# Optimization experiments

Hardware: AMD Instinct MI355X
Metric: run time of the kernel (lower is better)

## Reference

```python
import jax, jax.numpy as jnp
import numpy as np

D_MODEL = 1024
N_HEADS = 16
HEAD_DIM = D_MODEL // N_HEADS
MAX_LEN = 2048
BATCH = 2
SEQ = 2048


def setup_inputs() -> dict:
    key = jax.random.key(0)
    ks = jax.random.split(key, 6)
    std = 1.0 / np.sqrt(D_MODEL)
    x = jax.random.normal(ks[0], (BATCH, SEQ, D_MODEL), dtype=jnp.float32)
    Wqkv = jax.random.uniform(ks[1], (D_MODEL, 3 * D_MODEL), minval=-std, maxval=std, dtype=jnp.float32)
    bqkv = jax.random.uniform(ks[2], (3 * D_MODEL,), minval=-std, maxval=std, dtype=jnp.float32)
    Wout = jax.random.uniform(ks[3], (D_MODEL, D_MODEL), minval=-std, maxval=std, dtype=jnp.float32)
    bout = jax.random.uniform(ks[4], (D_MODEL,), minval=-std, maxval=std, dtype=jnp.float32)
    rel_pos_bias = 0.02 * jax.random.normal(ks[5], (2 * MAX_LEN - 1,), dtype=jnp.float32)
    return {"x": x, "Wqkv": Wqkv, "bqkv": bqkv, "Wout": Wout, "bout": bout, "rel_pos_bias": rel_pos_bias}


def reference(x, Wqkv, bqkv, Wout, bout, rel_pos_bias):
    B, S, _ = x.shape
    scale = HEAD_DIM ** -0.5
    qkv = x @ Wqkv + bqkv                       # [B,S,3*dm]
    qkv = qkv.reshape(B, S, 3, N_HEADS, HEAD_DIM)
    qkv = jnp.transpose(qkv, (2, 0, 3, 1, 4))   # [3,B,H,S,D]
    q, k, v = qkv[0], qkv[1], qkv[2]
    scores = jnp.einsum('bhqd,bhkd->bhqk', q, k) * scale
    pos = jnp.arange(S)
    rel = jnp.clip(pos[:, None] - pos[None, :] + (MAX_LEN - 1), 0, 2 * MAX_LEN - 2)
    scores = scores + rel_pos_bias[rel][None, None]  # bias shared over batch & heads
    probs = jax.nn.softmax(scores, axis=-1)
    out = jnp.einsum('bhqk,bhkd->bhqd', probs, v)    # [B,H,S,D]
    out = jnp.transpose(out, (0, 2, 1, 3)).reshape(B, S, D_MODEL)
    return out @ Wout + bout
```

## Files before the change

kernel.cpp:

```cpp
#include <hip/hip_runtime.h>
#include <cmath>

#define B_ 2
#define S_ 2048
#define H_ 16
#define D_ 64
#define DM 1024

typedef unsigned short u16;
using short8 = __attribute__((ext_vector_type(8))) short;
using f32x4  = __attribute__((ext_vector_type(4))) float;
using f32x16 = __attribute__((ext_vector_type(16))) float;
using i32x4  = __attribute__((ext_vector_type(4))) int;

__device__ __forceinline__ u16 f32_to_bf16(float f) {
    unsigned int u = __float_as_uint(f);
    u += 0x7fffu + ((u >> 16) & 1u);
    return (u16)(u >> 16);
}

__device__ __forceinline__ float exp2_fast(float x) {
    float r;
    asm("v_exp_f32 %0, %1" : "=v"(r) : "v"(x));
    return r;
}

__device__ __forceinline__ int cvt_pk_bf16(float lo, float hi) {
    int r;
    asm("v_cvt_pk_bf16_f32 %0, %1, %2" : "=v"(r) : "v"(lo), "v"(hi));
    return r;
}

__device__ __forceinline__ void gl_lds16(const void* src, void* dst) {
    __builtin_amdgcn_global_load_lds(
        (const __attribute__((address_space(1))) unsigned int*)src,
        (__attribute__((address_space(3))) unsigned int*)dst, 16, 0, 0);
}

__device__ __forceinline__ f32x16 mfma32(short8 a, short8 b, f32x16 c) {
    return __builtin_amdgcn_mfma_f32_32x32x16_bf16(a, b, c, 0, 0, 0);
}

__global__ __launch_bounds__(256) void relattn_prep(
    const float* __restrict__ x, const float* __restrict__ Wqkv,
    const float* __restrict__ Wout, const float* __restrict__ relb,
    u16* __restrict__ xb, u16* __restrict__ WqkvT, u16* __restrict__ WoutT,
    float* __restrict__ relb2)
{
    __shared__ float T[64][65];
    const int tid = threadIdx.x;
    int blk = blockIdx.x;
    if (blk >= 3072) {
        int i0 = ((blk - 3072) * 256 + tid) * 4;
#pragma unroll
        for (int j = 0; j < 4; ++j)
            if (i0 + j < 2 * 2048 - 1)
                relb2[i0 + j] = relb[i0 + j] * 1.44269504f;
        return;
    }
    if (blk < 2048) {
        size_t base = ((size_t)blk * 256 + tid) * 8;
        float4 v0 = *(const float4*)(x + base);
        float4 v1 = *(const float4*)(x + base + 4);
        ushort4 p0 = make_ushort4(f32_to_bf16(v0.x), f32_to_bf16(v0.y),
                                  f32_to_bf16(v0.z), f32_to_bf16(v0.w));
        ushort4 p1 = make_ushort4(f32_to_bf16(v1.x), f32_to_bf16(v1.y),
                                  f32_to_bf16(v1.z), f32_to_bf16(v1.w));
        *(ushort4*)(xb + base) = p0;
        *(ushort4*)(xb + base + 4) = p1;
        return;
    }
    int id = blk - 2048;
    const float* in; u16* outp; int R, C;
    if (id < 768) { in = Wqkv; outp = WqkvT; R = 1024; C = 3072; }
    else          { id -= 768; in = Wout;  outp = WoutT; R = 1024; C = 1024; }
    const int tpr = C >> 6;
    const int r0 = (id / tpr) << 6, c0 = (id % tpr) << 6;
#pragma unroll
    for (int it = 0; it < 4; ++it) {
        int e = tid + it * 256;
        int row = e >> 4, c4 = (e & 15) << 2;
        float4 v = *(const float4*)(in + (size_t)(r0 + row) * C + c0 + c4);
        T[row][c4 + 0] = v.x; T[row][c4 + 1] = v.y;
        T[row][c4 + 2] = v.z; T[row][c4 + 3] = v.w;
    }
    __syncthreads();
#pragma unroll
    for (int it = 0; it < 4; ++it) {
        int e = tid + it * 256;
        int crow = e >> 4, r4 = (e & 15) << 2;
        ushort4 pk = make_ushort4(f32_to_bf16(T[r4 + 0][crow]), f32_to_bf16(T[r4 + 1][crow]),
                                  f32_to_bf16(T[r4 + 2][crow]), f32_to_bf16(T[r4 + 3][crow]));
        *(ushort4*)(outp + (size_t)(c0 + crow) * R + r0 + r4) = pk;
    }
}

__global__ __launch_bounds__(256) void relattn_gemm_qkv(
    const u16* __restrict__ A, const u16* __restrict__ Bm,
    const float* __restrict__ bias, u16* __restrict__ qk, u16* __restrict__ Vt)
{
    __shared__ alignas(16) unsigned char AsB[16384];
    __shared__ alignas(16) unsigned char BsB[16384];
    const int tid = threadIdx.x;
    const int w = tid >> 6, l = tid & 63, ln = l & 15, hi = l >> 4;
    const int wr = w >> 1, wc = w & 1;
    const int row0 = blockIdx.y * 128, col0 = blockIdx.x * 128;
    const char* Ab = (const char*)A;
    const char* Bb = (const char*)Bm;

    f32x4 acc[4][4] = {};
    for (int step = 0; step < 16; ++step) {
        __syncthreads();
#pragma unroll
        for (int it = 0; it < 4; ++it) {
            int dsto = it * 4096 + w * 1024;
            int o = dsto + l * 16;
            int row = o >> 7;
            int swz = (o & 127) ^ ((row & 7) << 4);
            gl_lds16(Ab + (size_t)(row0 + row) * 2048 + step * 128 + swz, AsB + dsto);
            gl_lds16(Bb + (size_t)(col0 + row) * 2048 + step * 128 + swz, BsB + dsto);
        }
        __syncthreads();
#pragma unroll
        for (int kk = 0; kk < 2; ++kk) {
            short8 a[4], b[4];
            const int kb = hi * 16 + kk * 64;
#pragma unroll
            for (int m = 0; m < 4; ++m) {
                int row = wr * 64 + m * 16 + ln;
                a[m] = *(const short8*)(AsB + row * 128 + (kb ^ ((row & 7) << 4)));
            }
#pragma unroll
            for (int n = 0; n < 4; ++n) {
                int row = wc * 64 + n * 16 + ln;
                b[n] = *(const short8*)(BsB + row * 128 + (kb ^ ((row & 7) << 4)));
            }
#pragma unroll
            for (int m = 0; m < 4; ++m)
#pragma unroll
                for (int n = 0; n < 4; ++n)
                    acc[m][n] = __builtin_amdgcn_mfma_f32_16x16x32_bf16(a[m], b[n], acc[m][n], 0, 0, 0);
        }
    }

    const int t = col0 >> 10;
    const int bb = row0 >> 11;
    if (t < 2) {
#pragma unroll
        for (int n = 0; n < 4; ++n) {
            int c = col0 + wc * 64 + n * 16 + ln;
            int h = (c >> 6) & 15, d = c & 63;
            float bv = bias[c];
            u16* plane = qk + (size_t)((t * B_ + bb) * H_ + h) * S_ * D_;
#pragma unroll
            for (int m = 0; m < 4; ++m)
#pragma unroll
                for (int r = 0; r < 4; ++r) {
                    int s = (row0 + wr * 64 + m * 16 + hi * 4 + r) & (S_ - 1);
                    plane[(size_t)s * D_ + d] = f32_to_bf16(acc[m][n][r] + bv);
                }
        }
    } else {
#pragma unroll
        for (int n = 0; n < 4; ++n) {
            int c = col0 + wc * 64 + n * 16 + ln;
            int h = (c >> 6) & 15, d = c & 63;
            float bv = bias[c];
            u16* vrow = Vt + (size_t)((bb * H_ + h) * D_ + d) * S_;
#pragma unroll
            for (int m = 0; m < 4; ++m) {
                int s = (row0 + wr * 64 + m * 16 + hi * 4) & (S_ - 1);
                ushort4 pk = make_ushort4(f32_to_bf16(acc[m][n][0] + bv),
                                          f32_to_bf16(acc[m][n][1] + bv),
                                          f32_to_bf16(acc[m][n][2] + bv),
                                          f32_to_bf16(acc[m][n][3] + bv));
                *(ushort4*)(vrow + s) = pk;
            }
        }
    }
}

__global__ __launch_bounds__(512, 4) void relattn_attn(
    const u16* __restrict__ qk, const u16* __restrict__ Vt,
    const float* __restrict__ relb2, u16* __restrict__ aout)
{
    __shared__ alignas(16) unsigned char Lds[65536];
    const int tid = threadIdx.x;
    const int w = tid >> 6, l = tid & 63;
    const int wg = w & 3, g = w >> 2;
    const int l31 = l & 31, h2 = l >> 5;
    const int qt = blockIdx.x, bh = blockIdx.y;
    const int bb = bh >> 4;
    const char* qpl = (const char*)(qk + (size_t)bh * (S_ * D_));
    const char* kpl = (const char*)(qk + (size_t)(B_ * H_ + bh) * (S_ * D_));
    const char* vpl = (const char*)(Vt + (size_t)bh * (D_ * S_));
    unsigned char* GB = Lds + g * 32768;

    const int q0 = qt * 128 + wg * 32;
    const int qrow = q0 + l31;
    const int kvbase = g * 1024;

    short8 qf[4];
#pragma unroll
    for (int kd = 0; kd < 4; ++kd)
        qf[kd] = *(const short8*)(qpl + (size_t)qrow * 128 + kd * 32 + h2 * 16);

    f32x16 O0 = {}, O1 = {};
    float mrun = -1e30f, lrun = 0.f;

    {
#pragma unroll
        for (int it = 0; it < 2; ++it) {
            int dsto = it * 4096 + wg * 1024;
            int o = dsto + l * 16;
            int row = o >> 7;
            int swz = (o & 127) ^ ((row & 7) << 4);
            gl_lds16(kpl + (size_t)(kvbase + row) * 128 + swz, GB + dsto);
            gl_lds16(vpl + (size_t)row * (S_ * 2) + kvbase * 2 + swz, GB + 8192 + dsto);
        }
    }
    __syncthreads();

    for (int kt = 0; kt < 16; ++kt) {
        const int buf = kt & 1;
        const unsigned char* KB = GB + buf * 16384;
        const unsigned char* VB = KB + 8192;
        const int kv0 = kvbase + kt * 64;

        if (kt < 15) {
#pragma unroll
            for (int it = 0; it < 2; ++it) {
                int dsto = it * 4096 + wg * 1024;
                int o = dsto + l * 16;
                int row = o >> 7;
                int swz = (o & 127) ^ ((row & 7) << 4);
                unsigned char* db = GB + (buf ^ 1) * 16384 + dsto;
                gl_lds16(kpl + (size_t)(kv0 + 64 + row) * 128 + swz, db);
                gl_lds16(vpl + (size_t)row * (S_ * 2) + (kv0 + 64) * 2 + swz, db + 8192);
            }
        }

        f32x16 s0 = {}, s1 = {};
#pragma unroll
        for (int kd = 0; kd < 4; ++kd) {
            int kbyte = kd * 32 + h2 * 16;
            int sw = (l31 & 7) << 4;
            short8 k0 = *(const short8*)(KB + l31 * 128 + (kbyte ^ sw));
            short8 k1 = *(const short8*)(KB + (32 + l31) * 128 + (kbyte ^ sw));
            s0 = mfma32(k0, qf[kd], s0);
            s1 = mfma32(k1, qf[kd], s1);
        }

        const float SC2 = 0.125f * 1.44269504f;
        const float* bp = relb2 + (qrow - kv0 - 4 * h2 + 2047);
#pragma unroll
        for (int rq = 0; rq < 4; ++rq)
#pragma unroll
            for (int j = 0; j < 4; ++j) {
                s0[rq * 4 + j] = s0[rq * 4 + j] * SC2 + bp[-(8 * rq + j)];
                s1[rq * 4 + j] = s1[rq * 4 + j] * SC2 + bp[-(32 + 8 * rq + j)];
            }

        float tm = -1e30f;
#pragma unroll
        for (int r = 0; r < 16; ++r) {
            tm = fmaxf(tm, s0[r]);
            tm = fmaxf(tm, s1[r]);
        }
        tm = fmaxf(tm, __shfl_xor(tm, 32));
        float nm = fmaxf(mrun, tm);
        float al = exp2_fast(mrun - nm);
        mrun = nm;
        float ps = 0.f;
#pragma unroll
        for (int r = 0; r < 16; ++r) { s0[r] = exp2_fast(s0[r] - nm); ps += s0[r]; }
#pragma unroll
        for (int r = 0; r < 16; ++r) { s1[r] = exp2_fast(s1[r] - nm); ps += s1[r]; }
        ps += __shfl_xor(ps, 32);
        lrun = lrun * al + ps;
#pragma unroll
        for (int r = 0; r < 16; ++r) { O0[r] *= al; O1[r] *= al; }

#pragma unroll
        for (int ts = 0; ts < 4; ++ts) {
            float p0, p1, p2, p3, p4, p5, p6, p7;
            if (ts == 0)      { p0=s0[0];  p1=s0[1];  p2=s0[2];  p3=s0[3];  p4=s0[4];  p5=s0[5];  p6=s0[6];  p7=s0[7]; }
            else if (ts == 1) { p0=s0[8];  p1=s0[9];  p2=s0[10]; p3=s0[11]; p4=s0[12]; p5=s0[13]; p6=s0[14]; p7=s0[15]; }
            else if (ts == 2) { p0=s1[0];  p1=s1[1];  p2=s1[2];  p3=s1[3];  p4=s1[4];  p5=s1[5];  p6=s1[6];  p7=s1[7]; }
            else              { p0=s1[8];  p1=s1[9];  p2=s1[10]; p3=s1[11]; p4=s1[12]; p5=s1[13]; p6=s1[14]; p7=s1[15]; }
            int c01 = cvt_pk_bf16(p0, p1), c23 = cvt_pk_bf16(p2, p3);
            int c45 = cvt_pk_bf16(p4, p5), c67 = cvt_pk_bf16(p6, p7);
            int px01 = __shfl_xor(c01, 32), px23 = __shfl_xor(c23, 32);
            int px45 = __shfl_xor(c45, 32), px67 = __shfl_xor(c67, 32);
            i32x4 pw;
            pw[0] = h2 ? px45 : c01;
            pw[1] = h2 ? px67 : c23;
            pw[2] = h2 ? c45 : px01;
            pw[3] = h2 ? c67 : px23;
            short8 pb = __builtin_bit_cast(short8, pw);
            int vbyte = ts * 32 + h2 * 16;
            int sw = (l31 & 7) << 4;
            short8 v0 = *(const short8*)(VB + l31 * 128 + (vbyte ^ sw));
            short8 v1 = *(const short8*)(VB + (32 + l31) * 128 + (vbyte ^ sw));
            O0 = mfma32(v0, pb, O0);
            O1 = mfma32(v1, pb, O1);
        }
        __syncthreads();
    }

    {
        float* PO = (float*)(Lds + wg * 8704);
        float* PM = (float*)(Lds + wg * 8704 + 8192);
        float* PL = (float*)(Lds + wg * 8704 + 8448);
        if (g == 1) {
#pragma unroll
            for (int r = 0; r < 16; ++r) {
                PO[l * 32 + r] = O0[r];
                PO[l * 32 + 16 + r] = O1[r];
            }
            PM[l] = mrun;
            PL[l] = lrun;
        }
        __syncthreads();
        if (g == 1) return;
        float m1v = PM[l], l1v = PL[l];
        float nm = fmaxf(mrun, m1v);
        float a0 = exp2_fast(mrun - nm), a1 = exp2_fast(m1v - nm);
        float lr = lrun * a0 + l1v * a1;
        float inv = 1.0f / lr;
        const float* src = PO + l * 32;
        u16* orow = aout + (size_t)(bb * S_ + qrow) * DM + (bh & 15) * 64 + 4 * h2;
#pragma unroll
        for (int gq = 0; gq < 4; ++gq) {
            ushort4 w0, w1;
            float o00 = (O0[4*gq+0] * a0 + src[4*gq+0] * a1) * inv;
            float o01 = (O0[4*gq+1] * a0 + src[4*gq+1] * a1) * inv;
            float o02 = (O0[4*gq+2] * a0 + src[4*gq+2] * a1) * inv;
            float o03 = (O0[4*gq+3] * a0 + src[4*gq+3] * a1) * inv;
            float o10 = (O1[4*gq+0] * a0 + src[16+4*gq+0] * a1) * inv;
            float o11 = (O1[4*gq+1] * a0 + src[16+4*gq+1] * a1) * inv;
            float o12 = (O1[4*gq+2] * a0 + src[16+4*gq+2] * a1) * inv;
            float o13 = (O1[4*gq+3] * a0 + src[16+4*gq+3] * a1) * inv;
            w0 = make_ushort4(f32_to_bf16(o00), f32_to_bf16(o01), f32_to_bf16(o02), f32_to_bf16(o03));
            w1 = make_ushort4(f32_to_bf16(o10), f32_to_bf16(o11), f32_to_bf16(o12), f32_to_bf16(o13));
            *(ushort4*)(orow + 8 * gq) = w0;
            *(ushort4*)(orow + 32 + 8 * gq) = w1;
        }
    }
}

__global__ __launch_bounds__(256) void relattn_gemm_out(
    const u16* __restrict__ A, const u16* __restrict__ Bm,
    const float* __restrict__ bias, float* __restrict__ out)
{
    __shared__ alignas(16) unsigned char AsB[16384];
    __shared__ alignas(16) unsigned char BsB[16384];
    const int tid = threadIdx.x;
    const int w = tid >> 6, l = tid & 63, ln = l & 15, hi = l >> 4;
    const int wr = w >> 1, wc = w & 1;
    const int row0 = blockIdx.y * 128, col0 = blockIdx.x * 128;
    const char* Ab = (const char*)A;
    const char* Bb = (const char*)Bm;

    f32x4 acc[4][4] = {};
    for (int step = 0; step < 16; ++step) {
        __syncthreads();
#pragma unroll
        for (int it = 0; it < 4; ++it) {
            int dsto = it * 4096 + w * 1024;
            int o = dsto + l * 16;
            int row = o >> 7;
            int swz = (o & 127) ^ ((row & 7) << 4);
            gl_lds16(Ab + (size_t)(row0 + row) * 2048 + step * 128 + swz, AsB + dsto);
            gl_lds16(Bb + (size_t)(col0 + row) * 2048 + step * 128 + swz, BsB + dsto);
        }
        __syncthreads();
#pragma unroll
        for (int kk = 0; kk < 2; ++kk) {
            short8 a[4], b[4];
            const int kb = hi * 16 + kk * 64;
#pragma unroll
            for (int m = 0; m < 4; ++m) {
                int row = wr * 64 + m * 16 + ln;
                a[m] = *(const short8*)(AsB + row * 128 + (kb ^ ((row & 7) << 4)));
            }
#pragma unroll
            for (int n = 0; n < 4; ++n) {
                int row = wc * 64 + n * 16 + ln;
                b[n] = *(const short8*)(BsB + row * 128 + (kb ^ ((row & 7) << 4)));
            }
#pragma unroll
            for (int m = 0; m < 4; ++m)
#pragma unroll
                for (int n = 0; n < 4; ++n)
                    acc[m][n] = __builtin_amdgcn_mfma_f32_16x16x32_bf16(a[m], b[n], acc[m][n], 0, 0, 0);
        }
    }

#pragma unroll
    for (int n = 0; n < 4; ++n) {
        int c = col0 + wc * 64 + n * 16 + ln;
        float bv = bias[c];
#pragma unroll
        for (int m = 0; m < 4; ++m)
#pragma unroll
            for (int r = 0; r < 4; ++r) {
                int row = row0 + wr * 64 + m * 16 + hi * 4 + r;
                out[(size_t)row * DM + c] = acc[m][n][r] + bv;
            }
    }
}

extern "C" void kernel_launch(void* const* d_in, const int* in_sizes, int n_in,
                              void* d_out, int out_size, void* d_ws, size_t ws_size,
                              hipStream_t stream) {
    const float* x    = (const float*)d_in[0];
    const float* Wqkv = (const float*)d_in[1];
    const float* bqkv = (const float*)d_in[2];
    const float* Wout = (const float*)d_in[3];
    const float* bout = (const float*)d_in[4];
    const float* relb = (const float*)d_in[5];
    float* out = (float*)d_out;

    u16* ws    = (u16*)d_ws;
    u16* xb    = ws;
    u16* WqkvT = xb + 4194304;
    u16* WoutT = WqkvT + 3145728;
    u16* qkpl  = WoutT + 1048576;
    u16* Vt    = qkpl + 8388608;
    u16* aout  = Vt + 4194304;
    float* relb2 = (float*)(aout + 4194304);

    relattn_prep<<<3076, 256, 0, stream>>>(x, Wqkv, Wout, relb, xb, WqkvT, WoutT, relb2);
    relattn_gemm_qkv<<<dim3(24, 32), 256, 0, stream>>>(xb, WqkvT, bqkv, qkpl, Vt);
    relattn_attn<<<dim3(16, 32), 512, 0, stream>>>(qkpl, Vt, relb2, aout);
    relattn_gemm_out<<<dim3(8, 32), 256, 0, stream>>>(aout, WoutT, bout, out);
}
```

Measured before the change: 138.6 us.

## Add lazy softmax rescale, vectorized bias loads, and MFMA priority hints

Moves the relative-position bias loads ahead of the QK MFMAs as vector loads, so they overlap with the matrix work. It also adds a conditional (lazy) online-softmax rescale that skips rescaling O and l unless the max grows by more than 8 in log2 units. Other changes are tree-shaped max and sum reductions, s_setprio around the MFMA blocks, and a folded normalisation in the epilogue. The lazy rescale lets exp values reach up to 2^8, which adds some bf16/fp32 range risk, and the priority hints may or may not help the wave scheduling.

Result: slower. 149.1 us (+7.6%).

```diff
diff --git a/kernel.cpp b/kernel.cpp
--- a/kernel.cpp
+++ b/kernel.cpp
@@ -12,6 +12,7 @@
 using f32x4  = __attribute__((ext_vector_type(4))) float;
 using f32x16 = __attribute__((ext_vector_type(16))) float;
 using i32x4  = __attribute__((ext_vector_type(4))) int;
+typedef float uf4 __attribute__((ext_vector_type(4), aligned(4)));
 
 __device__ __forceinline__ u16 f32_to_bf16(float f) {
     unsigned int u = __float_as_uint(f);
@@ -240,7 +241,16 @@
             }
         }
 
+        const float* bp0 = relb2 + (qrow - kv0 - 4 * h2 + 2047);
+        uf4 bv0[4], bv1[4];
+#pragma unroll
+        for (int rq = 0; rq < 4; ++rq) {
+            bv0[rq] = *(const uf4*)(bp0 - 8 * rq - 3);
+            bv1[rq] = *(const uf4*)(bp0 - 32 - 8 * rq - 3);
+        }
+
         f32x16 s0 = {}, s1 = {};
+        __builtin_amdgcn_s_setprio(1);
 #pragma unroll
         for (int kd = 0; kd < 4; ++kd) {
             int kbyte = kd * 32 + h2 * 16;
@@ -250,37 +260,51 @@
             s0 = mfma32(k0, qf[kd], s0);
             s1 = mfma32(k1, qf[kd], s1);
         }
+        __builtin_amdgcn_s_setprio(0);
 
         const float SC2 = 0.125f * 1.44269504f;
-        const float* bp = relb2 + (qrow - kv0 - 4 * h2 + 2047);
 #pragma unroll
         for (int rq = 0; rq < 4; ++rq)
 #pragma unroll
             for (int j = 0; j < 4; ++j) {
-                s0[rq * 4 + j] = s0[rq * 4 + j] * SC2 + bp[-(8 * rq + j)];
-                s1[rq * 4 + j] = s1[rq * 4 + j] * SC2 + bp[-(32 + 8 * rq + j)];
-            }
-
-        float tm = -1e30f;
-#pragma unroll
-        for (int r = 0; r < 16; ++r) {
-            tm = fmaxf(tm, s0[r]);
-            tm = fmaxf(tm, s1[r]);
-        }
+                s0[rq * 4 + j] = s0[rq * 4 + j] * SC2 + bv0[rq][3 - j];
+                s1[rq * 4 + j] = s1[rq * 4 + j] * SC2 + bv1[rq][3 - j];
+            }
+
+        float a0 = fmaxf(fmaxf(s0[0], s0[1]), fmaxf(s0[2], s0[3]));
+        float a1 = fmaxf(fmaxf(s0[4], s0[5]), fmaxf(s0[6], s0[7]));
+        float a2 = fmaxf(fmaxf(s0[8], s0[9]), fmaxf(s0[10], s0[11]));
+        float a3 = fmaxf(fmaxf(s0[12], s0[13]), fmaxf(s0[14], s0[15]));
+        float a4 = fmaxf(fmaxf(s1[0], s1[1]), fmaxf(s1[2], s1[3]));
+        float a5 = fmaxf(fmaxf(s1[4], s1[5]), fmaxf(s1[6], s1[7]));
+        float a6 = fmaxf(fmaxf(s1[8], s1[9]), fmaxf(s1[10], s1[11]));
+        float a7 = fmaxf(fmaxf(s1[12], s1[13]), fmaxf(s1[14], s1[15]));
+        float tm = fmaxf(fmaxf(fmaxf(a0, a1), fmaxf(a2, a3)),
+                         fmaxf(fmaxf(a4, a5), fmaxf(a6, a7)));
         tm = fmaxf(tm, __shfl_xor(tm, 32));
-        float nm = fmaxf(mrun, tm);
-        float al = exp2_fast(mrun - nm);
-        mrun = nm;
-        float ps = 0.f;
-#pragma unroll
-        for (int r = 0; r < 16; ++r) { s0[r] = exp2_fast(s0[r] - nm); ps += s0[r]; }
-#pragma unroll
-        for (int r = 0; r < 16; ++r) { s1[r] = exp2_fast(s1[r] - nm); ps += s1[r]; }
+
+        if (!__all(tm - mrun <= 8.0f)) {
+            float nm = fmaxf(mrun, tm);
+            float al = exp2_fast(mrun - nm);
+            mrun = nm;
+            lrun *= al;
+#pragma unroll
+            for (int r = 0; r < 16; ++r) { O0[r] *= al; O1[r] *= al; }
+        }
+
+#pragma unroll
+        for (int r = 0; r < 16; ++r) s0[r] = exp2_fast(s0[r] - mrun);
+#pragma unroll
+        for (int r = 0; r < 16; ++r) s1[r] = exp2_fast(s1[r] - mrun);
+        float q0s = ((s0[0] + s0[1]) + (s0[2] + s0[3])) + ((s0[4] + s0[5]) + (s0[6] + s0[7]));
+        float q1s = ((s0[8] + s0[9]) + (s0[10] + s0[11])) + ((s0[12] + s0[13]) + (s0[14] + s0[15]));
+        float q2s = ((s1[0] + s1[1]) + (s1[2] + s1[3])) + ((s1[4] + s1[5]) + (s1[6] + s1[7]));
+        float q3s = ((s1[8] + s1[9]) + (s1[10] + s1[11])) + ((s1[12] + s1[13]) + (s1[14] + s1[15]));
+        float ps = (q0s + q1s) + (q2s + q3s);
         ps += __shfl_xor(ps, 32);
-        lrun = lrun * al + ps;
-#pragma unroll
-        for (int r = 0; r < 16; ++r) { O0[r] *= al; O1[r] *= al; }
-
+        lrun += ps;
+
+        __builtin_amdgcn_s_setprio(1);
 #pragma unroll
         for (int ts = 0; ts < 4; ++ts) {
             float p0, p1, p2, p3, p4, p5, p6, p7;
@@ -305,6 +329,7 @@
             O0 = mfma32(v0, pb, O0);
             O1 = mfma32(v1, pb, O1);
         }
+        __builtin_amdgcn_s_setprio(0);
         __syncthreads();
     }
 
@@ -325,24 +350,24 @@
         if (g == 1) return;
         float m1v = PM[l], l1v = PL[l];
         float nm = fmaxf(mrun, m1v);
-        float a0 = exp2_fast(mrun - nm), a1 = exp2_fast(m1v - nm);
-        float lr = lrun * a0 + l1v * a1;
+        float a0m = exp2_fast(mrun - nm), a1m = exp2_fast(m1v - nm);
+        float lr = lrun * a0m + l1v * a1m;
         float inv = 1.0f / lr;
+        float f0 = a0m * inv, f1 = a1m * inv;
         const float* src = PO + l * 32;
         u16* orow = aout + (size_t)(bb * S_ + qrow) * DM + (bh & 15) * 64 + 4 * h2;
 #pragma unroll
         for (int gq = 0; gq < 4; ++gq) {
-            ushort4 w0, w1;
-            float o00 = (O0[4*gq+0] * a0 + src[4*gq+0] * a1) * inv;
-            float o01 = (O0[4*gq+1] * a0 + src[4*gq+1] * a1) * inv;
-            float o02 = (O0[4*gq+2] * a0 + src[4*gq+2] * a1) * inv;
-            float o03 = (O0[4*gq+3] * a0 + src[4*gq+3] * a1) * inv;
-            float o10 = (O1[4*gq+0] * a0 + src[16+4*gq+0] * a1) * inv;
-            float o11 = (O1[4*gq+1] * a0 + src[16+4*gq+1] * a1) * inv;
-            float o12 = (O1[4*gq+2] * a0 + src[16+4*gq+2] * a1) * inv;
-            float o13 = (O1[4*gq+3] * a0 + src[16+4*gq+3] * a1) * inv;
-            w0 = make_ushort4(f32_to_bf16(o00), f32_to_bf16(o01), f32_to_bf16(o02), f32_to_bf16(o03));
-            w1 = make_ushort4(f32_to_bf16(o10), f32_to_bf16(o11), f32_to_bf16(o12), f32_to_bf16(o13));
+            float o00 = O0[4*gq+0] * f0 + src[4*gq+0] * f1;
+            float o01 = O0[4*gq+1] * f0 + src[4*gq+1] * f1;
+            float o02 = O0[4*gq+2] * f0 + src[4*gq+2] * f1;
+            float o03 = O0[4*gq+3] * f0 + src[4*gq+3] * f1;
+            float o10 = O1[4*gq+0] * f0 + src[16+4*gq+0] * f1;
+            float o11 = O1[4*gq+1] * f0 + src[16+4*gq+1] * f1;
+            float o12 = O1[4*gq+2] * f0 + src[16+4*gq+2] * f1;
+            float o13 = O1[4*gq+3] * f0 + src[16+4*gq+3] * f1;
+            ushort4 w0 = make_ushort4(f32_to_bf16(o00), f32_to_bf16(o01), f32_to_bf16(o02), f32_to_bf16(o03));
+            ushort4 w1 = make_ushort4(f32_to_bf16(o10), f32_to_bf16(o11), f32_to_bf16(o12), f32_to_bf16(o13));
             *(ushort4*)(orow + 8 * gq) = w0;
             *(ushort4*)(orow + 32 + 8 * gq) = w1;
         }
```
